# Kernel optimization log

Hardware: AMD Instinct MI355X
Metric: run time of the kernel (lower is better)

Reference implementation:

```python
import jax, jax.numpy as jnp
import numpy as np


def setup_inputs() -> dict:
    key = jax.random.key(0)
    ks = jax.random.split(key, 7)
    B, C, W, H = 4, 256, 128, 128
    s = 1.0 / np.sqrt(C)
    return {
        "x": jax.random.normal(ks[0], (B, C, W, H), dtype=jnp.float32),
        "wq": jax.random.normal(ks[1], (C, C), dtype=jnp.float32) * s,
        "bq": jax.random.normal(ks[2], (C,), dtype=jnp.float32) * s,
        "wk": jax.random.normal(ks[3], (C, C), dtype=jnp.float32) * s,
        "bk": jax.random.normal(ks[4], (C,), dtype=jnp.float32) * s,
        "wv": jax.random.normal(ks[5], (C, C), dtype=jnp.float32) * s,
        "bv": jax.random.normal(ks[6], (C,), dtype=jnp.float32) * s,
    }


def reference(x, wq, bq, wk, bk, wv, bv):
    B, C, W, H = x.shape
    N = W * H
    xf = x.reshape(B, C, N)  # flatten spatial: (B, C, N)
    # 1x1 convs are channel-mixing GEMMs: out[b,o,n] = sum_c w[o,c] x[b,c,n] + b[o]
    q = jnp.einsum('oc,bcn->bon', wq, xf) + bq[:, None]
    k = jnp.einsum('oc,bcn->bon', wk, xf) + bk[:, None]
    v = jnp.einsum('oc,bcn->bon', wv, xf) + bv[:, None]
    # channel-channel energy: (B, C, C)
    energy = jnp.einsum('bcn,bdn->bcd', q, k) / jnp.sqrt(jnp.float32(N))
    attention = jax.nn.softmax(energy, axis=-1)
    out = jnp.einsum('bcd,bdn->bcn', attention, v)
    return out.reshape(B, C, W, H) + x
```

## Files before the change

### kernel.cpp

```cpp
#include <hip/hip_runtime.h>
#include <stdint.h>

#define BB 4
#define CC 256
#define NN 16384

typedef unsigned short u16;
typedef __attribute__((ext_vector_type(8))) __bf16 bf16x8;
typedef __attribute__((ext_vector_type(4))) float f32x4;

__device__ __forceinline__ u16 f2bf(float f) {
  union { float f; uint32_t u; } c;
  c.f = f;
  uint32_t u = c.u;
  return (u16)((u + 0x7fffu + ((u >> 16) & 1u)) >> 16);
}

__device__ __forceinline__ void g2l16(const u16* g, u16* l) {
  __builtin_amdgcn_global_load_lds((__attribute__((address_space(1))) void*)g,
                                   (__attribute__((address_space(3))) void*)l, 16, 0, 0);
}

__device__ __forceinline__ void stage128x32(const u16* src, int stride, u16* lds, int tid) {
  int r = tid >> 2;
  int c = (tid & 3) << 3;
  g2l16(src + (size_t)r * stride + c, lds + r * 32 + c);
  g2l16(src + (size_t)(r + 64) * stride + c, lds + (r + 64) * 32 + c);
}

__device__ __forceinline__ void stage128x32_w8(const u16* src, int stride, u16* lds, int tid) {
  int r = tid >> 2;
  int c = (tid & 3) << 3;
  g2l16(src + (size_t)r * stride + c, lds + r * 32 + c);
}

__device__ __forceinline__ void stage256x32_w8(const u16* src, int stride, u16* lds, int tid) {
  int r = tid >> 2;
  int c = (tid & 3) << 3;
  g2l16(src + (size_t)r * stride + c, lds + r * 32 + c);
  g2l16(src + (size_t)(r + 128) * stride + c, lds + (r + 128) * 32 + c);
}

__device__ __forceinline__ void mfma_tile(const u16* As, const u16* Bs, int mb, int nb,
                                          int l16, int q8, f32x4 acc[4][4]) {
  bf16x8 af[4], bf[4];
#pragma unroll
  for (int i = 0; i < 4; i++) af[i] = *(const bf16x8*)&As[(mb + i * 16 + l16) * 32 + q8];
#pragma unroll
  for (int i = 0; i < 4; i++) bf[i] = *(const bf16x8*)&Bs[(nb + i * 16 + l16) * 32 + q8];
#pragma unroll
  for (int i = 0; i < 4; i++)
#pragma unroll
    for (int j = 0; j < 4; j++)
      acc[i][j] = __builtin_amdgcn_mfma_f32_16x16x32_bf16(af[i], bf[j], acc[i][j], 0, 0, 0);
}

__global__ __launch_bounds__(256) void prep_kernel(const float* __restrict__ x,
                                                   u16* __restrict__ xb,
                                                   u16* __restrict__ xbT,
                                                   float* __restrict__ s) {
  __shared__ float t[64][65];
  __shared__ float rs[64][4];
  int n0 = blockIdx.x * 64, c0 = blockIdx.y * 64, bz = blockIdx.z;
  int tid = threadIdx.x;
  int rr0 = tid >> 4, q4 = (tid & 15) * 4;
  const float* xs = x + ((size_t)bz * CC + c0) * NN + n0;
  u16* xbp = xb + ((size_t)bz * CC + c0) * NN + n0;
#pragma unroll
  for (int cc = rr0; cc < 64; cc += 16) {
    float4 v = *(const float4*)&xs[(size_t)cc * NN + q4];
    t[cc][q4] = v.x; t[cc][q4 + 1] = v.y; t[cc][q4 + 2] = v.z; t[cc][q4 + 3] = v.w;
    union { u16 h[4]; uint2 u; } pk;
    pk.h[0] = f2bf(v.x); pk.h[1] = f2bf(v.y); pk.h[2] = f2bf(v.z); pk.h[3] = f2bf(v.w);
    *(uint2*)&xbp[(size_t)cc * NN + q4] = pk.u;
  }
  __syncthreads();
  {
    int r = tid >> 2, q = tid & 3;
    float p = 0.f;
#pragma unroll
    for (int i = 0; i < 16; i++) p += t[r][q * 16 + i];
    rs[r][q] = p;
  }
  u16* od = xbT + ((size_t)bz * NN + n0) * CC + c0;
#pragma unroll
  for (int nn = rr0; nn < 64; nn += 16) {
    union { u16 h[4]; uint2 u; } pk;
    pk.h[0] = f2bf(t[q4][nn]); pk.h[1] = f2bf(t[q4 + 1][nn]);
    pk.h[2] = f2bf(t[q4 + 2][nn]); pk.h[3] = f2bf(t[q4 + 3][nn]);
    *(uint2*)&od[(size_t)nn * CC + q4] = pk.u;
  }
  __syncthreads();
  if (tid < 64)
    atomicAdd(&s[bz * CC + c0 + tid], rs[tid][0] + rs[tid][1] + rs[tid][2] + rs[tid][3]);
}

__global__ __launch_bounds__(256) void gram_kernel(const u16* __restrict__ xb,
                                                   float* __restrict__ G) {
  __shared__ u16 As[2][128 * 32], Bs[2][128 * 32];
  int tid = threadIdx.x;
  int c0 = (blockIdx.x >> 1) * 128, d0 = (blockIdx.x & 1) * 128;
  int sl = blockIdx.y, bz = blockIdx.z;
  const u16* A = xb + ((size_t)bz * CC + c0) * NN + sl * 512;
  const u16* Bt = xb + ((size_t)bz * CC + d0) * NN + sl * 512;
  f32x4 acc[4][4] = {};
  int wave = tid >> 6, lane = tid & 63;
  int mb = (wave >> 1) * 64, nb = (wave & 1) * 64;
  int quad = lane >> 4, l16 = lane & 15, q8 = quad * 8;
  for (int kk = 0; kk < 512; kk += 64) {
    stage128x32(A + kk, NN, As[0], tid);
    stage128x32(A + kk + 32, NN, As[1], tid);
    stage128x32(Bt + kk, NN, Bs[0], tid);
    stage128x32(Bt + kk + 32, NN, Bs[1], tid);
    __syncthreads();
    mfma_tile(As[0], Bs[0], mb, nb, l16, q8, acc);
    mfma_tile(As[1], Bs[1], mb, nb, l16, q8, acc);
    __syncthreads();
  }
  float* g = G + (size_t)bz * CC * CC;
#pragma unroll
  for (int i = 0; i < 4; i++)
#pragma unroll
    for (int j = 0; j < 4; j++)
#pragma unroll
      for (int r = 0; r < 4; r++)
        atomicAdd(&g[(size_t)(c0 + mb + i * 16 + quad * 4 + r) * CC + d0 + nb + j * 16 + l16],
                  acc[i][j][r]);
}

__global__ __launch_bounds__(256) void ru_kernel(const float* __restrict__ Wq,
                                                 const float* __restrict__ G,
                                                 const float* __restrict__ s,
                                                 const float* __restrict__ bq,
                                                 float* __restrict__ R) {
  __shared__ float As[32][33], Bs2[32][33];
  int t = threadIdx.x;
  int c0 = blockIdx.x * 32, o0 = blockIdx.y * 32, b = blockIdx.z;
  const float* Ap = Wq + (size_t)o0 * CC;
  const float* Bp = G + (size_t)b * CC * CC + c0;
  float acc[2][2] = {};
  int r = t >> 3, c4 = (t & 7) * 4;
  int tr = t >> 4, tc = t & 15;
  for (int kk = 0; kk < CC; kk += 32) {
    float4 av = *(const float4*)&Ap[(size_t)r * CC + kk + c4];
    float4 bv = *(const float4*)&Bp[(size_t)(kk + r) * CC + c4];
    As[r][c4] = av.x; As[r][c4 + 1] = av.y; As[r][c4 + 2] = av.z; As[r][c4 + 3] = av.w;
    Bs2[r][c4] = bv.x; Bs2[r][c4 + 1] = bv.y; Bs2[r][c4 + 2] = bv.z; Bs2[r][c4 + 3] = bv.w;
    __syncthreads();
#pragma unroll
    for (int k = 0; k < 32; k++) {
      float a0 = As[tr * 2][k], a1 = As[tr * 2 + 1][k];
      float b0 = Bs2[k][tc * 2], b1 = Bs2[k][tc * 2 + 1];
      acc[0][0] += a0 * b0; acc[0][1] += a0 * b1;
      acc[1][0] += a1 * b0; acc[1][1] += a1 * b1;
    }
    __syncthreads();
  }
#pragma unroll
  for (int i = 0; i < 2; i++)
#pragma unroll
    for (int j = 0; j < 2; j++) {
      int o = o0 + tr * 2 + i, c = c0 + tc * 2 + j;
      R[(size_t)b * CC * CC + (size_t)o * CC + c] = acc[i][j] + bq[o] * s[b * CC + c];
    }
}

__global__ __launch_bounds__(256) void esb_kernel(
    const float* __restrict__ R, const float* __restrict__ Wq,
    const float* __restrict__ Wk, const float* __restrict__ s,
    const float* __restrict__ bq, const float* __restrict__ bk,
    const float* __restrict__ bv,
    float* __restrict__ att, float* __restrict__ bo) {
  __shared__ float upS[8];
  __shared__ float red[4][8];
  __shared__ float red2[4][16];
  int t = threadIdx.x;
  int o0 = blockIdx.x * 8, b = blockIdx.y;
  {
    int o = t >> 5, l = t & 31;
    const float* wqr = Wq + (size_t)(o0 + o) * CC;
    const float* sb = s + b * CC;
    float p = 0.f;
#pragma unroll
    for (int k = 0; k < 8; k++) p += wqr[l + 32 * k] * sb[l + 32 * k];
#pragma unroll
    for (int d = 16; d > 0; d >>= 1) p += __shfl_xor(p, d, 32);
    if (l == 0) upS[o] = p + 16384.f * bq[o0 + o];
  }
  __syncthreads();
  float bkp = bk[t], bvp = bv[t];
  float acc[8];
#pragma unroll
  for (int o = 0; o < 8; o++) acc[o] = upS[o] * bkp;
  const float* wkr = Wk + (size_t)t * CC;
  const float* Rb = R + ((size_t)b * CC + o0) * CC;
  for (int c = 0; c < CC; c += 4) {
    float4 wv4 = *(const float4*)&wkr[c];
#pragma unroll
    for (int o = 0; o < 8; o++) {
      float4 rv = *(const float4*)&Rb[(size_t)o * CC + c];
      acc[o] += rv.x * wv4.x + rv.y * wv4.y + rv.z * wv4.z + rv.w * wv4.w;
    }
  }
#pragma unroll
  for (int o = 0; o < 8; o++) acc[o] *= 0.0078125f;
  int wv = t >> 6, ln = t & 63;
#pragma unroll
  for (int o = 0; o < 8; o++) {
    float v = acc[o];
#pragma unroll
    for (int d = 32; d > 0; d >>= 1) v = fmaxf(v, __shfl_xor(v, d, 64));
    if (ln == 0) red[wv][o] = v;
  }
  __syncthreads();
  float m[8];
#pragma unroll
  for (int o = 0; o < 8; o++)
    m[o] = fmaxf(fmaxf(red[0][o], red[1][o]), fmaxf(red[2][o], red[3][o]));
#pragma unroll
  for (int o = 0; o < 8; o++) acc[o] = __expf(acc[o] - m[o]);
#pragma unroll
  for (int o = 0; o < 8; o++) {
    float v = acc[o], w2 = acc[o] * bvp;
#pragma unroll
    for (int d = 32; d > 0; d >>= 1) {
      v += __shfl_xor(v, d, 64);
      w2 += __shfl_xor(w2, d, 64);
    }
    if (ln == 0) { red2[wv][o] = v; red2[wv][o + 8] = w2; }
  }
  __syncthreads();
  float* ar = att + ((size_t)b * CC + o0) * CC;
#pragma unroll
  for (int o = 0; o < 8; o++) {
    float ssum = red2[0][o] + red2[1][o] + red2[2][o] + red2[3][o];
    float inv = 1.f / ssum;
    ar[(size_t)o * CC + t] = acc[o] * inv;
    if (t == o) {
      float bsum = red2[0][o + 8] + red2[1][o + 8] + red2[2][o + 8] + red2[3][o + 8];
      bo[b * CC + o0 + o] = bsum * inv;
    }
  }
}

__global__ __launch_bounds__(256) void nn_Mv_kernel(const float* __restrict__ att,
                                                    const float* __restrict__ Wv,
                                                    u16* __restrict__ Mvb) {
  __shared__ float As[32][33], Bs2[32][33];
  int t = threadIdx.x;
  int c0 = blockIdx.x * 32, o0 = blockIdx.y * 32, b = blockIdx.z;
  const float* Ap = att + (size_t)b * CC * CC + (size_t)o0 * CC;
  const float* Bp = Wv + c0;
  float acc[2][2] = {};
  int r = t >> 3, c4 = (t & 7) * 4;
  int tr = t >> 4, tc = t & 15;
  for (int kk = 0; kk < CC; kk += 32) {
    float4 av = *(const float4*)&Ap[(size_t)r * CC + kk + c4];
    float4 bv = *(const float4*)&Bp[(size_t)(kk + r) * CC + c4];
    As[r][c4] = av.x; As[r][c4 + 1] = av.y; As[r][c4 + 2] = av.z; As[r][c4 + 3] = av.w;
    Bs2[r][c4] = bv.x; Bs2[r][c4 + 1] = bv.y; Bs2[r][c4 + 2] = bv.z; Bs2[r][c4 + 3] = bv.w;
    __syncthreads();
#pragma unroll
    for (int k = 0; k < 32; k++) {
      float a0 = As[tr * 2][k], a1 = As[tr * 2 + 1][k];
      float b0 = Bs2[k][tc * 2], b1 = Bs2[k][tc * 2 + 1];
      acc[0][0] += a0 * b0; acc[0][1] += a0 * b1;
      acc[1][0] += a1 * b0; acc[1][1] += a1 * b1;
    }
    __syncthreads();
  }
#pragma unroll
  for (int i = 0; i < 2; i++)
#pragma unroll
    for (int j = 0; j < 2; j++)
      Mvb[(size_t)b * CC * CC + (size_t)(o0 + tr * 2 + i) * CC + c0 + tc * 2 + j] =
          f2bf(acc[i][j]);
}

__global__ __launch_bounds__(512) void out_kernel(const u16* __restrict__ Mvb,
                                                  const u16* __restrict__ xbT,
                                                  const float* __restrict__ bo,
                                                  const float* __restrict__ x,
                                                  float* __restrict__ out) {
  __shared__ u16 As[2][128 * 32], Bs[2][256 * 32];
  int tid = threadIdx.x;
  int n0 = blockIdx.x * 256, m0 = blockIdx.y * 128, bz = blockIdx.z;
  const u16* A = Mvb + (size_t)bz * CC * CC + (size_t)m0 * CC;
  const u16* Bt = xbT + ((size_t)bz * NN + n0) * CC;
  f32x4 acc[4][4] = {};
  int wave = tid >> 6, lane = tid & 63;
  int mb = (wave & 1) * 64, nb = (wave >> 1) * 64;
  int quad = lane >> 4, l16 = lane & 15, q8 = quad * 8;
  for (int kk = 0; kk < CC; kk += 64) {
    stage128x32_w8(A + kk, CC, As[0], tid);
    stage128x32_w8(A + kk + 32, CC, As[1], tid);
    stage256x32_w8(Bt + kk, CC, Bs[0], tid);
    stage256x32_w8(Bt + kk + 32, CC, Bs[1], tid);
    __syncthreads();
    mfma_tile(As[0], Bs[0], mb, nb, l16, q8, acc);
    mfma_tile(As[1], Bs[1], mb, nb, l16, q8, acc);
    __syncthreads();
  }
#pragma unroll
  for (int i = 0; i < 4; i++)
#pragma unroll
    for (int r = 0; r < 4; r++) {
      int cg = m0 + mb + i * 16 + quad * 4 + r;
      float bc = bo[bz * CC + cg];
#pragma unroll
      for (int j = 0; j < 4; j++) {
        int ng = n0 + nb + j * 16 + l16;
        size_t idx = ((size_t)bz * CC + cg) * NN + ng;
        out[idx] = acc[i][j][r] + bc + x[idx];
      }
    }
}

extern "C" void kernel_launch(void* const* d_in, const int* in_sizes, int n_in,
                              void* d_out, int out_size, void* d_ws, size_t ws_size,
                              hipStream_t stream) {
  (void)in_sizes; (void)n_in; (void)out_size; (void)ws_size;
  const float* x = (const float*)d_in[0];
  const float* wq = (const float*)d_in[1];
  const float* bq = (const float*)d_in[2];
  const float* wk = (const float*)d_in[3];
  const float* bk = (const float*)d_in[4];
  const float* wv = (const float*)d_in[5];
  const float* bv = (const float*)d_in[6];
  float* out = (float*)d_out;

  char* ws = (char*)d_ws;
  u16* xb    = (u16*)(ws + 0);
  u16* xbT   = (u16*)(ws + 33554432);
  float* G   = (float*)(ws + 67108864);
  float* s   = (float*)(ws + 68157440);
  float* R   = (float*)(ws + 68161536);
  float* att = (float*)(ws + 69210112);
  u16* Mvb   = (u16*)(ws + 70258688);
  float* bo  = (float*)(ws + 70782976);

  hipMemsetAsync(G, 0, 1048576 + 4096, stream);
  prep_kernel<<<dim3(NN / 64, CC / 64, BB), 256, 0, stream>>>(x, xb, xbT, s);
  gram_kernel<<<dim3(4, 32, BB), 256, 0, stream>>>(xb, G);
  ru_kernel<<<dim3(8, 8, BB), 256, 0, stream>>>(wq, G, s, bq, R);
  esb_kernel<<<dim3(32, BB), 256, 0, stream>>>(R, wq, wk, s, bq, bk, bv, att, bo);
  nn_Mv_kernel<<<dim3(8, 8, BB), 256, 0, stream>>>(att, wv, Mvb);
  out_kernel<<<dim3(NN / 256, CC / 128, BB), 512, 0, stream>>>(Mvb, xbT, bo, x, out);
}
```

Measured before the change: 247.5 us.

## Replace atomics with split-K partial buffers and fuse middle small GEMMs into one kernel

Gram and channel-sum partials are now written to per-slice buffers and summed by a separate reduce kernel instead of float atomics, which also removes the memset. The ru, esb and Mv kernels are fused into one mid kernel. Each block handles two query rows and keeps R and the attention rows in shared memory, so the R and att intermediates no longer go through global memory. In exchange it writes and reads a 32 MB partial buffer and launches 512 small blocks with scalar strided loops.

```diff
diff --git a/kernel.cpp b/kernel.cpp
--- a/kernel.cpp
+++ b/kernel.cpp
@@ -4,6 +4,7 @@
 #define BB 4
 #define CC 256
 #define NN 16384
+#define NSL 32
 
 typedef unsigned short u16;
 typedef __attribute__((ext_vector_type(8))) __bf16 bf16x8;
@@ -58,7 +59,7 @@
 __global__ __launch_bounds__(256) void prep_kernel(const float* __restrict__ x,
                                                    u16* __restrict__ xb,
                                                    u16* __restrict__ xbT,
-                                                   float* __restrict__ s) {
+                                                   float* __restrict__ s_part) {
   __shared__ float t[64][65];
   __shared__ float rs[64][4];
   int n0 = blockIdx.x * 64, c0 = blockIdx.y * 64, bz = blockIdx.z;
@@ -92,11 +93,12 @@
   }
   __syncthreads();
   if (tid < 64)
-    atomicAdd(&s[bz * CC + c0 + tid], rs[tid][0] + rs[tid][1] + rs[tid][2] + rs[tid][3]);
+    s_part[((size_t)bz * 256 + blockIdx.x) * CC + c0 + tid] =
+        rs[tid][0] + rs[tid][1] + rs[tid][2] + rs[tid][3];
 }
 
 __global__ __launch_bounds__(256) void gram_kernel(const u16* __restrict__ xb,
-                                                   float* __restrict__ G) {
+                                                   float* __restrict__ Gp) {
   __shared__ u16 As[2][128 * 32], Bs[2][128 * 32];
   int tid = threadIdx.x;
   int c0 = (blockIdx.x >> 1) * 128, d0 = (blockIdx.x & 1) * 128;
@@ -117,164 +119,135 @@
     mfma_tile(As[1], Bs[1], mb, nb, l16, q8, acc);
     __syncthreads();
   }
-  float* g = G + (size_t)bz * CC * CC;
+  float* gp = Gp + ((size_t)sl * BB + bz) * CC * CC;
 #pragma unroll
   for (int i = 0; i < 4; i++)
 #pragma unroll
     for (int j = 0; j < 4; j++)
 #pragma unroll
       for (int r = 0; r < 4; r++)
-        atomicAdd(&g[(size_t)(c0 + mb + i * 16 + quad * 4 + r) * CC + d0 + nb + j * 16 + l16],
-                  acc[i][j][r]);
-}
-
-__global__ __launch_bounds__(256) void ru_kernel(const float* __restrict__ Wq,
-                                                 const float* __restrict__ G,
-                                                 const float* __restrict__ s,
-                                                 const float* __restrict__ bq,
-                                                 float* __restrict__ R) {
-  __shared__ float As[32][33], Bs2[32][33];
-  int t = threadIdx.x;
-  int c0 = blockIdx.x * 32, o0 = blockIdx.y * 32, b = blockIdx.z;
-  const float* Ap = Wq + (size_t)o0 * CC;
-  const float* Bp = G + (size_t)b * CC * CC + c0;
-  float acc[2][2] = {};
-  int r = t >> 3, c4 = (t & 7) * 4;
-  int tr = t >> 4, tc = t & 15;
-  for (int kk = 0; kk < CC; kk += 32) {
-    float4 av = *(const float4*)&Ap[(size_t)r * CC + kk + c4];
-    float4 bv = *(const float4*)&Bp[(size_t)(kk + r) * CC + c4];
-    As[r][c4] = av.x; As[r][c4 + 1] = av.y; As[r][c4 + 2] = av.z; As[r][c4 + 3] = av.w;
-    Bs2[r][c4] = bv.x; Bs2[r][c4 + 1] = bv.y; Bs2[r][c4 + 2] = bv.z; Bs2[r][c4 + 3] = bv.w;
-    __syncthreads();
-#pragma unroll
-    for (int k = 0; k < 32; k++) {
-      float a0 = As[tr * 2][k], a1 = As[tr * 2 + 1][k];
-      float b0 = Bs2[k][tc * 2], b1 = Bs2[k][tc * 2 + 1];
-      acc[0][0] += a0 * b0; acc[0][1] += a0 * b1;
-      acc[1][0] += a1 * b0; acc[1][1] += a1 * b1;
-    }
-    __syncthreads();
-  }
-#pragma unroll
-  for (int i = 0; i < 2; i++)
-#pragma unroll
-    for (int j = 0; j < 2; j++) {
-      int o = o0 + tr * 2 + i, c = c0 + tc * 2 + j;
-      R[(size_t)b * CC * CC + (size_t)o * CC + c] = acc[i][j] + bq[o] * s[b * CC + c];
-    }
-}
-
-__global__ __launch_bounds__(256) void esb_kernel(
-    const float* __restrict__ R, const float* __restrict__ Wq,
-    const float* __restrict__ Wk, const float* __restrict__ s,
+        gp[(size_t)(c0 + mb + i * 16 + quad * 4 + r) * CC + d0 + nb + j * 16 + l16] =
+            acc[i][j][r];
+}
+
+__global__ __launch_bounds__(256) void reduce_kernel(const float* __restrict__ Gp,
+                                                     const float* __restrict__ s_part,
+                                                     float* __restrict__ G,
+                                                     float* __restrict__ s) {
+  int t = threadIdx.x, blk = blockIdx.x;
+  size_t base = ((size_t)blk * 256 + t) * 4;
+  float ax = 0.f, ay = 0.f, az = 0.f, aw = 0.f;
+#pragma unroll 8
+  for (int sl = 0; sl < NSL; sl++) {
+    float4 v = *(const float4*)&Gp[(size_t)sl * (BB * CC * CC) + base];
+    ax += v.x; ay += v.y; az += v.z; aw += v.w;
+  }
+  float4 o; o.x = ax; o.y = ay; o.z = az; o.w = aw;
+  *(float4*)&G[base] = o;
+  if (blk < BB) {
+    float a = 0.f;
+#pragma unroll 8
+    for (int nt = 0; nt < 256; nt++) a += s_part[((size_t)blk * 256 + nt) * CC + t];
+    s[blk * CC + t] = a;
+  }
+}
+
+__global__ __launch_bounds__(256) void mid_kernel(
+    const float* __restrict__ G, const float* __restrict__ s,
+    const float* __restrict__ Wq, const float* __restrict__ Wk,
+    const float* __restrict__ Wv,
     const float* __restrict__ bq, const float* __restrict__ bk,
     const float* __restrict__ bv,
-    float* __restrict__ att, float* __restrict__ bo) {
-  __shared__ float upS[8];
-  __shared__ float red[4][8];
-  __shared__ float red2[4][16];
+    u16* __restrict__ Mvb, float* __restrict__ bo) {
+  __shared__ float sS[CC];
+  __shared__ float rS[2][CC];
+  __shared__ float attS[2][CC];
+  __shared__ float redA[2][4], redB[2][4], redC[2][4], redD[2][4];
   int t = threadIdx.x;
-  int o0 = blockIdx.x * 8, b = blockIdx.y;
-  {
-    int o = t >> 5, l = t & 31;
-    const float* wqr = Wq + (size_t)(o0 + o) * CC;
-    const float* sb = s + b * CC;
-    float p = 0.f;
-#pragma unroll
-    for (int k = 0; k < 8; k++) p += wqr[l + 32 * k] * sb[l + 32 * k];
-#pragma unroll
-    for (int d = 16; d > 0; d >>= 1) p += __shfl_xor(p, d, 32);
-    if (l == 0) upS[o] = p + 16384.f * bq[o0 + o];
-  }
-  __syncthreads();
-  float bkp = bk[t], bvp = bv[t];
-  float acc[8];
-#pragma unroll
-  for (int o = 0; o < 8; o++) acc[o] = upS[o] * bkp;
+  int o0 = blockIdx.x * 2, b = blockIdx.y;
+  int wv = t >> 6, ln = t & 63;
+  sS[t] = s[b * CC + t];
+  __syncthreads();
+  float p0 = Wq[(size_t)o0 * CC + t] * sS[t];
+  float p1 = Wq[(size_t)(o0 + 1) * CC + t] * sS[t];
+#pragma unroll
+  for (int d = 32; d > 0; d >>= 1) {
+    p0 += __shfl_xor(p0, d, 64);
+    p1 += __shfl_xor(p1, d, 64);
+  }
+  if (ln == 0) { redA[0][wv] = p0; redA[1][wv] = p1; }
+  __syncthreads();
+  float up0 = redA[0][0] + redA[0][1] + redA[0][2] + redA[0][3] + 16384.f * bq[o0];
+  float up1 = redA[1][0] + redA[1][1] + redA[1][2] + redA[1][3] + 16384.f * bq[o0 + 1];
+  const float* Gb = G + (size_t)b * CC * CC;
+  const float* wq0 = Wq + (size_t)o0 * CC;
+  const float* wq1 = wq0 + CC;
+  float r0 = bq[o0] * sS[t], r1 = bq[o0 + 1] * sS[t];
+#pragma unroll 8
+  for (int d = 0; d < CC; d++) {
+    float g = Gb[d * CC + t];
+    r0 += wq0[d] * g;
+    r1 += wq1[d] * g;
+  }
+  rS[0][t] = r0;
+  rS[1][t] = r1;
+  __syncthreads();
+  float e0 = up0 * bk[t], e1 = up1 * bk[t];
   const float* wkr = Wk + (size_t)t * CC;
-  const float* Rb = R + ((size_t)b * CC + o0) * CC;
+#pragma unroll 4
   for (int c = 0; c < CC; c += 4) {
-    float4 wv4 = *(const float4*)&wkr[c];
-#pragma unroll
-    for (int o = 0; o < 8; o++) {
-      float4 rv = *(const float4*)&Rb[(size_t)o * CC + c];
-      acc[o] += rv.x * wv4.x + rv.y * wv4.y + rv.z * wv4.z + rv.w * wv4.w;
-    }
-  }
-#pragma unroll
-  for (int o = 0; o < 8; o++) acc[o] *= 0.0078125f;
-  int wv = t >> 6, ln = t & 63;
-#pragma unroll
-  for (int o = 0; o < 8; o++) {
-    float v = acc[o];
-#pragma unroll
-    for (int d = 32; d > 0; d >>= 1) v = fmaxf(v, __shfl_xor(v, d, 64));
-    if (ln == 0) red[wv][o] = v;
-  }
-  __syncthreads();
-  float m[8];
-#pragma unroll
-  for (int o = 0; o < 8; o++)
-    m[o] = fmaxf(fmaxf(red[0][o], red[1][o]), fmaxf(red[2][o], red[3][o]));
-#pragma unroll
-  for (int o = 0; o < 8; o++) acc[o] = __expf(acc[o] - m[o]);
-#pragma unroll
-  for (int o = 0; o < 8; o++) {
-    float v = acc[o], w2 = acc[o] * bvp;
-#pragma unroll
-    for (int d = 32; d > 0; d >>= 1) {
-      v += __shfl_xor(v, d, 64);
-      w2 += __shfl_xor(w2, d, 64);
-    }
-    if (ln == 0) { red2[wv][o] = v; red2[wv][o + 8] = w2; }
-  }
-  __syncthreads();
-  float* ar = att + ((size_t)b * CC + o0) * CC;
-#pragma unroll
-  for (int o = 0; o < 8; o++) {
-    float ssum = red2[0][o] + red2[1][o] + red2[2][o] + red2[3][o];
-    float inv = 1.f / ssum;
-    ar[(size_t)o * CC + t] = acc[o] * inv;
-    if (t == o) {
-      float bsum = red2[0][o + 8] + red2[1][o + 8] + red2[2][o + 8] + red2[3][o + 8];
-      bo[b * CC + o0 + o] = bsum * inv;
-    }
-  }
-}
-
-__global__ __launch_bounds__(256) void nn_Mv_kernel(const float* __restrict__ att,
-                                                    const float* __restrict__ Wv,
-                                                    u16* __restrict__ Mvb) {
-  __shared__ float As[32][33], Bs2[32][33];
-  int t = threadIdx.x;
-  int c0 = blockIdx.x * 32, o0 = blockIdx.y * 32, b = blockIdx.z;
-  const float* Ap = att + (size_t)b * CC * CC + (size_t)o0 * CC;
-  const float* Bp = Wv + c0;
-  float acc[2][2] = {};
-  int r = t >> 3, c4 = (t & 7) * 4;
-  int tr = t >> 4, tc = t & 15;
-  for (int kk = 0; kk < CC; kk += 32) {
-    float4 av = *(const float4*)&Ap[(size_t)r * CC + kk + c4];
-    float4 bv = *(const float4*)&Bp[(size_t)(kk + r) * CC + c4];
-    As[r][c4] = av.x; As[r][c4 + 1] = av.y; As[r][c4 + 2] = av.z; As[r][c4 + 3] = av.w;
-    Bs2[r][c4] = bv.x; Bs2[r][c4 + 1] = bv.y; Bs2[r][c4 + 2] = bv.z; Bs2[r][c4 + 3] = bv.w;
-    __syncthreads();
-#pragma unroll
-    for (int k = 0; k < 32; k++) {
-      float a0 = As[tr * 2][k], a1 = As[tr * 2 + 1][k];
-      float b0 = Bs2[k][tc * 2], b1 = Bs2[k][tc * 2 + 1];
-      acc[0][0] += a0 * b0; acc[0][1] += a0 * b1;
-      acc[1][0] += a1 * b0; acc[1][1] += a1 * b1;
-    }
-    __syncthreads();
-  }
-#pragma unroll
-  for (int i = 0; i < 2; i++)
-#pragma unroll
-    for (int j = 0; j < 2; j++)
-      Mvb[(size_t)b * CC * CC + (size_t)(o0 + tr * 2 + i) * CC + c0 + tc * 2 + j] =
-          f2bf(acc[i][j]);
+    float4 w4 = *(const float4*)&wkr[c];
+    float4 ra = *(const float4*)&rS[0][c];
+    float4 rb = *(const float4*)&rS[1][c];
+    e0 += ra.x * w4.x + ra.y * w4.y + ra.z * w4.z + ra.w * w4.w;
+    e1 += rb.x * w4.x + rb.y * w4.y + rb.z * w4.z + rb.w * w4.w;
+  }
+  e0 *= 0.0078125f;
+  e1 *= 0.0078125f;
+  float m0 = e0, m1 = e1;
+#pragma unroll
+  for (int d = 32; d > 0; d >>= 1) {
+    m0 = fmaxf(m0, __shfl_xor(m0, d, 64));
+    m1 = fmaxf(m1, __shfl_xor(m1, d, 64));
+  }
+  if (ln == 0) { redB[0][wv] = m0; redB[1][wv] = m1; }
+  __syncthreads();
+  m0 = fmaxf(fmaxf(redB[0][0], redB[0][1]), fmaxf(redB[0][2], redB[0][3]));
+  m1 = fmaxf(fmaxf(redB[1][0], redB[1][1]), fmaxf(redB[1][2], redB[1][3]));
+  e0 = __expf(e0 - m0);
+  e1 = __expf(e1 - m1);
+  float s0 = e0, s1 = e1;
+#pragma unroll
+  for (int d = 32; d > 0; d >>= 1) {
+    s0 += __shfl_xor(s0, d, 64);
+    s1 += __shfl_xor(s1, d, 64);
+  }
+  if (ln == 0) { redC[0][wv] = s0; redC[1][wv] = s1; }
+  __syncthreads();
+  float inv0 = 1.f / (redC[0][0] + redC[0][1] + redC[0][2] + redC[0][3]);
+  float inv1 = 1.f / (redC[1][0] + redC[1][1] + redC[1][2] + redC[1][3]);
+  float a0 = e0 * inv0, a1 = e1 * inv1;
+  attS[0][t] = a0;
+  attS[1][t] = a1;
+  float b0 = a0 * bv[t], b1 = a1 * bv[t];
+#pragma unroll
+  for (int d = 32; d > 0; d >>= 1) {
+    b0 += __shfl_xor(b0, d, 64);
+    b1 += __shfl_xor(b1, d, 64);
+  }
+  if (ln == 0) { redD[0][wv] = b0; redD[1][wv] = b1; }
+  __syncthreads();
+  if (t == 0) bo[b * CC + o0] = redD[0][0] + redD[0][1] + redD[0][2] + redD[0][3];
+  if (t == 1) bo[b * CC + o0 + 1] = redD[1][0] + redD[1][1] + redD[1][2] + redD[1][3];
+  float mv0 = 0.f, mv1 = 0.f;
+#pragma unroll 8
+  for (int d = 0; d < CC; d++) {
+    float w = Wv[d * CC + t];
+    mv0 += attS[0][d] * w;
+    mv1 += attS[1][d] * w;
+  }
+  Mvb[((size_t)b * CC + o0) * CC + t] = f2bf(mv0);
+  Mvb[((size_t)b * CC + o0 + 1) * CC + t] = f2bf(mv1);
 }
 
 __global__ __launch_bounds__(512) void out_kernel(const u16* __restrict__ Mvb,
@@ -330,20 +303,18 @@
   float* out = (float*)d_out;
 
   char* ws = (char*)d_ws;
-  u16* xb    = (u16*)(ws + 0);
-  u16* xbT   = (u16*)(ws + 33554432);
-  float* G   = (float*)(ws + 67108864);
-  float* s   = (float*)(ws + 68157440);
-  float* R   = (float*)(ws + 68161536);
-  float* att = (float*)(ws + 69210112);
-  u16* Mvb   = (u16*)(ws + 70258688);
-  float* bo  = (float*)(ws + 70782976);
-
-  hipMemsetAsync(G, 0, 1048576 + 4096, stream);
-  prep_kernel<<<dim3(NN / 64, CC / 64, BB), 256, 0, stream>>>(x, xb, xbT, s);
-  gram_kernel<<<dim3(4, 32, BB), 256, 0, stream>>>(xb, G);
-  ru_kernel<<<dim3(8, 8, BB), 256, 0, stream>>>(wq, G, s, bq, R);
-  esb_kernel<<<dim3(32, BB), 256, 0, stream>>>(R, wq, wk, s, bq, bk, bv, att, bo);
-  nn_Mv_kernel<<<dim3(8, 8, BB), 256, 0, stream>>>(att, wv, Mvb);
+  u16* xb      = (u16*)(ws + 0);
+  u16* xbT     = (u16*)(ws + 33554432);
+  float* Gp    = (float*)(ws + 67108864);
+  float* G     = (float*)(ws + 100663296);
+  float* s_prt = (float*)(ws + 101711872);
+  float* s     = (float*)(ws + 102760448);
+  u16* Mvb     = (u16*)(ws + 102764544);
+  float* bo    = (float*)(ws + 103288832);
+
+  prep_kernel<<<dim3(NN / 64, CC / 64, BB), 256, 0, stream>>>(x, xb, xbT, s_prt);
+  gram_kernel<<<dim3(4, NSL, BB), 256, 0, stream>>>(xb, Gp);
+  reduce_kernel<<<256, 256, 0, stream>>>(Gp, s_prt, G, s);
+  mid_kernel<<<dim3(CC / 2, BB), 256, 0, stream>>>(G, s, wq, wk, wv, bq, bk, bv, Mvb, bo);
   out_kernel<<<dim3(NN / 256, CC / 128, BB), 512, 0, stream>>>(Mvb, xbT, bo, x, out);
 }
```

Measured after the change: 237.2 us. 4.2% less time.
